# Optimization experiments

Hardware: AMD Instinct MI355X
Metric: run time of the kernel (lower is better)

Reference implementation:

```python
import jax, jax.numpy as jnp
import numpy as np

NEG_SLOPE = 0.2  # PyG GATConv default negative_slope


def _add_self_loops(edge_index, num_nodes):
    # PyG GATConv add_self_loops=True default
    loop = jnp.arange(num_nodes, dtype=edge_index.dtype)
    src = jnp.concatenate([edge_index[0], loop])
    dst = jnp.concatenate([edge_index[1], loop])
    return src, dst


def _gat_layer(x, src, dst, W, att_src, att_dst, bias, heads, out_ch):
    """One PyG-style GATConv layer (concat=True).
    x: [N, F_in]; W: [F_in, heads*out_ch]; att_*: [heads, out_ch]; bias: [heads*out_ch].
    """
    N = x.shape[0]
    h = (x @ W).reshape(N, heads, out_ch)               # [N, H, C]
    a_src = jnp.einsum('nhc,hc->nh', h, att_src)        # [N, H]
    a_dst = jnp.einsum('nhc,hc->nh', h, att_dst)        # [N, H]
    logits = jax.nn.leaky_relu(a_src[src] + a_dst[dst], NEG_SLOPE)  # [E, H]
    # segment softmax over destination neighborhoods
    m = jax.ops.segment_max(logits, dst, num_segments=N)            # [N, H]
    e = jnp.exp(logits - m[dst])                                     # [E, H]
    s = jax.ops.segment_sum(e, dst, num_segments=N)                  # [N, H]
    alpha = e / s[dst]                                               # [E, H]
    # scatter-aggregate weighted source features
    out = jax.ops.segment_sum(alpha[:, :, None] * h[src], dst, num_segments=N)  # [N, H, C]
    return out.reshape(N, heads * out_ch) + bias


def setup_inputs() -> dict:
    key = jax.random.key(0)
    ks = jax.random.split(key, 10)
    N, E = 50000, 800000
    F_in, HID, H, NC = 128, 64, 4, 10
    x = jax.random.normal(ks[0], (N, F_in), dtype=jnp.float32)
    edge_index = jax.random.randint(ks[1], (2, E), 0, N, dtype=jnp.int64)
    sc1 = 1.0 / np.sqrt(F_in)
    sc2 = 1.0 / np.sqrt(HID * H)
    return {
        'x': x,
        'edge_index': edge_index,
        'W1': jax.random.normal(ks[2], (F_in, H * HID), dtype=jnp.float32) * sc1,
        'att_src1': jax.random.normal(ks[3], (H, HID), dtype=jnp.float32) * sc1,
        'att_dst1': jax.random.normal(ks[4], (H, HID), dtype=jnp.float32) * sc1,
        'b1': jnp.zeros((H * HID,), dtype=jnp.float32),
        'W2': jax.random.normal(ks[5], (H * HID, NC), dtype=jnp.float32) * sc2,
        'att_src2': jax.random.normal(ks[6], (1, NC), dtype=jnp.float32) * sc2,
        'att_dst2': jax.random.normal(ks[7], (1, NC), dtype=jnp.float32) * sc2,
        'b2': jnp.zeros((NC,), dtype=jnp.float32),
    }


def reference(x, edge_index, W1, att_src1, att_dst1, b1, W2, att_src2, att_dst2, b2):
    N = x.shape[0]
    src, dst = _add_self_loops(edge_index, N)
    h = _gat_layer(x, src, dst, W1, att_src1, att_dst1, b1, heads=4, out_ch=64)
    h = jax.nn.elu(h)
    out = _gat_layer(h, src, dst, W2, att_src2, att_dst2, b2, heads=1, out_ch=10)
    return out
```

## Files before the change

### kernel.cpp

```cpp
#include <hip/hip_runtime.h>
#include <hip/hip_fp16.h>
#include <math.h>

#define NEG_SLOPE 0.2f
#define LOG2E 1.44269504088896f

#if __has_builtin(__builtin_amdgcn_exp2f)
#define EXP2(x) __builtin_amdgcn_exp2f(x)
#else
#define EXP2(x) exp2f(x)
#endif

typedef _Float16 half8 __attribute__((ext_vector_type(8)));
typedef float floatx4 __attribute__((ext_vector_type(4)));

__global__ __launch_bounds__(256) void prep1(const float* __restrict__ W1,
                                             half8* __restrict__ Bpack,
                                             int* __restrict__ deg, int N) {
  if (blockIdx.x < 16) {
    int tid = blockIdx.x * 256 + threadIdx.x;
    int l = tid & 63;
    int ksnt = tid >> 6;
    int ks = ksnt & 3;
    int nt = ksnt >> 2;
    int col = nt * 16 + (l & 15);
    int krow = ks * 32 + (l >> 4) * 8;
    half8 v;
#pragma unroll
    for (int j = 0; j < 8; j++) v[j] = (_Float16)W1[(krow + j) * 256 + col];
    Bpack[tid] = v;
  } else {
    int i = (blockIdx.x - 16) * 256 + threadIdx.x;
    if (i < N) deg[i] = 0;
  }
}

__global__ __launch_bounds__(256) void phase2(
    const float* __restrict__ x, const half8* __restrict__ Bpack,
    const float* __restrict__ att_s, const float* __restrict__ att_d,
    unsigned char* __restrict__ h1q, float* __restrict__ hscale,
    float* __restrict__ a1s, float* __restrict__ a1d,
    const int* __restrict__ dst, int* __restrict__ deg, int* __restrict__ rank,
    int N, int E, int gemmBlocks, int histBlocks) {
  if ((int)blockIdx.x >= gemmBlocks) {
    int b = blockIdx.x - gemmBlocks;
    for (int e = b * 256 + threadIdx.x; e < E; e += histBlocks * 256)
      rank[e] = atomicAdd(deg + dst[e], 1);
    return;
  }
  const int wave = threadIdx.x >> 6, lane = threadIdx.x & 63;
  const int quad = lane >> 4, li = lane & 15;
  const int n0 = (blockIdx.x * 4 + wave) * 16;
  if (n0 >= N) return;
  floatx4 acc[16];
#pragma unroll
  for (int t = 0; t < 16; t++) acc[t] = (floatx4){0.f, 0.f, 0.f, 0.f};
  const float* xrow = x + (size_t)(n0 + li) * 128;
#pragma unroll
  for (int ks = 0; ks < 4; ks++) {
    float4 xa = *(const float4*)(xrow + ks * 32 + quad * 8);
    float4 xb = *(const float4*)(xrow + ks * 32 + quad * 8 + 4);
    half8 a;
    a[0] = (_Float16)xa.x; a[1] = (_Float16)xa.y;
    a[2] = (_Float16)xa.z; a[3] = (_Float16)xa.w;
    a[4] = (_Float16)xb.x; a[5] = (_Float16)xb.y;
    a[6] = (_Float16)xb.z; a[7] = (_Float16)xb.w;
#pragma unroll
    for (int nt = 0; nt < 16; nt++) {
      half8 b = Bpack[(nt * 4 + ks) * 64 + lane];
      acc[nt] = __builtin_amdgcn_mfma_f32_16x16x32_f16(a, b, acc[nt], 0, 0, 0);
    }
  }
#pragma unroll
  for (int r = 0; r < 4; r++) {
    float m = 0.f;
#pragma unroll
    for (int nt = 0; nt < 16; nt++) m = fmaxf(m, fabsf(acc[nt][r]));
#pragma unroll
    for (int off = 8; off > 0; off >>= 1) m = fmaxf(m, __shfl_xor(m, off, 16));
    m = fmaxf(m, 1e-8f);
    float inv = 127.0f / m;
    int node = n0 + quad * 4 + r;
    if (li == 0) hscale[node] = m * (1.0f / 127.0f);
#pragma unroll
    for (int nt = 0; nt < 16; nt++) {
      h1q[(size_t)node * 256 + nt * 16 + li] =
          (unsigned char)(int)(fmaf(acc[nt][r], inv, 128.5f));
    }
  }
  float as_f[16], ad_f[16];
#pragma unroll
  for (int nt = 0; nt < 16; nt++) {
    as_f[nt] = att_s[nt * 16 + li];
    ad_f[nt] = att_d[nt * 16 + li];
  }
#pragma unroll
  for (int r = 0; r < 4; r++) {
    int node = n0 + quad * 4 + r;
#pragma unroll
    for (int h = 0; h < 4; h++) {
      float vs = 0.f, vd = 0.f;
#pragma unroll
      for (int ntl = 0; ntl < 4; ntl++) {
        int nt = h * 4 + ntl;
        vs = fmaf(acc[nt][r], as_f[nt], vs);
        vd = fmaf(acc[nt][r], ad_f[nt], vd);
      }
#pragma unroll
      for (int off = 8; off > 0; off >>= 1) {
        vs += __shfl_down(vs, off, 16);
        vd += __shfl_down(vd, off, 16);
      }
      if (li == 0) {
        a1s[node * 4 + h] = vs * LOG2E;
        a1d[node * 4 + h] = vd * LOG2E;
      }
    }
  }
}

__global__ void scan_local(const int* __restrict__ deg, int* __restrict__ excl,
                           int* __restrict__ bsum, int N) {
  __shared__ int s[256];
  int i = blockIdx.x * 256 + threadIdx.x;
  int v = (i < N) ? deg[i] + 1 : 0;
  s[threadIdx.x] = v;
  __syncthreads();
  for (int off = 1; off < 256; off <<= 1) {
    int t = (threadIdx.x >= off) ? s[threadIdx.x - off] : 0;
    __syncthreads();
    s[threadIdx.x] += t;
    __syncthreads();
  }
  if (i < N) excl[i] = s[threadIdx.x] - v;
  if (threadIdx.x == 255) bsum[blockIdx.x] = s[255];
}

__global__ void scan_add2(const int* __restrict__ excl, const int* __restrict__ bsum,
                          int* __restrict__ rowptr, int* __restrict__ elist,
                          int N, int nb) {
  __shared__ int s[256];
  int v = (threadIdx.x < nb) ? bsum[threadIdx.x] : 0;
  s[threadIdx.x] = v;
  __syncthreads();
  for (int off = 1; off < 256; off <<= 1) {
    int t = (threadIdx.x >= off) ? s[threadIdx.x - off] : 0;
    __syncthreads();
    s[threadIdx.x] += t;
    __syncthreads();
  }
  __syncthreads();
  int base = (blockIdx.x > 0) ? s[blockIdx.x - 1] : 0;
  int i = blockIdx.x * 256 + threadIdx.x;
  if (i < N) {
    int r = excl[i] + base;
    rowptr[i] = r;
    elist[r] = i;
  }
  if (blockIdx.x == 0 && threadIdx.x == 0) rowptr[N] = s[nb - 1];
}

__global__ void scatter2(const int* __restrict__ src, const int* __restrict__ dst,
                         const int* __restrict__ rank, const int* __restrict__ rowptr,
                         int* __restrict__ elist, int E) {
  int e = blockIdx.x * 256 + threadIdx.x;
  if (e >= E) return;
  elist[rowptr[dst[e]] + 1 + rank[e]] = src[e];
}

__global__ __launch_bounds__(256) void agg1_fused(
    const int* __restrict__ rowptr, const int* __restrict__ elist,
    const unsigned char* __restrict__ h1q, const float* __restrict__ hscale,
    const float* __restrict__ a1s, const float* __restrict__ a1d,
    const float* __restrict__ b1, const float* __restrict__ W2,
    const float* __restrict__ as2, const float* __restrict__ ad2,
    __half* __restrict__ h2, float* __restrict__ a2s, float* __restrict__ a2d,
    int N) {
  __shared__ float w2s[64 * 41];
  __shared__ float cbuf[8][256];
  const int t = threadIdx.x;
  for (int i = t; i < 2560; i += 256) {
    int ch = i / 10, jj = i - ch * 10;
    w2s[(ch >> 2) * 41 + (ch & 3) * 10 + jj] = W2[i];
  }

  const int wave = t >> 6, lane = t & 63;
  const int half = lane >> 5, l32 = lane & 31;
  const int slot = wave * 2 + half;
  const int n = blockIdx.x * 8 + slot;
  const bool act = n < N;
  const int row = act ? rowptr[n] : 0;
  const int deg = act ? rowptr[n + 1] - row : 0;
  const int* el = elist + row;
  const int hidx = l32 >> 3;
  const float adh = act ? a1d[n * 4 + hidx] : 0.f;

  float den = 0.f, T = 0.f;
  float acc[8];
#pragma unroll
  for (int k = 0; k < 8; k++) acc[k] = 0.f;

  int j = 0;
  for (; j + 4 <= deg; j += 4) {
    int ss[4];
    float lv[4], sc[4];
    uint2 qv[4];
#pragma unroll
    for (int u = 0; u < 4; u++) ss[u] = el[j + u];
#pragma unroll
    for (int u = 0; u < 4; u++) {
      lv[u] = a1s[ss[u] * 4 + hidx];
      sc[u] = hscale[ss[u]];
      qv[u] = *(const uint2*)(h1q + (size_t)ss[u] * 256 + l32 * 8);
    }
#pragma unroll
    for (int u = 0; u < 4; u++) {
      float l = lv[u] + adh;
      float e = EXP2(fmaxf(l, NEG_SLOPE * l));
      den += e;
      float se = e * sc[u];
      T += se;
      unsigned int a = qv[u].x, b = qv[u].y;
      acc[0] = fmaf((float)(a & 0xffu), se, acc[0]);
      acc[1] = fmaf((float)((a >> 8) & 0xffu), se, acc[1]);
      acc[2] = fmaf((float)((a >> 16) & 0xffu), se, acc[2]);
      acc[3] = fmaf((float)(a >> 24), se, acc[3]);
      acc[4] = fmaf((float)(b & 0xffu), se, acc[4]);
      acc[5] = fmaf((float)((b >> 8) & 0xffu), se, acc[5]);
      acc[6] = fmaf((float)((b >> 16) & 0xffu), se, acc[6]);
      acc[7] = fmaf((float)(b >> 24), se, acc[7]);
    }
  }
  for (; j < deg; j++) {
    int s0 = el[j];
    float l0 = a1s[s0 * 4 + hidx] + adh;
    float sc0 = hscale[s0];
    uint2 q0 = *(const uint2*)(h1q + (size_t)s0 * 256 + l32 * 8);
    float e0 = EXP2(fmaxf(l0, NEG_SLOPE * l0));
    den += e0;
    float se = e0 * sc0;
    T += se;
    unsigned int a = q0.x, b = q0.y;
    acc[0] = fmaf((float)(a & 0xffu), se, acc[0]);
    acc[1] = fmaf((float)((a >> 8) & 0xffu), se, acc[1]);
    acc[2] = fmaf((float)((a >> 16) & 0xffu), se, acc[2]);
    acc[3] = fmaf((float)(a >> 24), se, acc[3]);
    acc[4] = fmaf((float)(b & 0xffu), se, acc[4]);
    acc[5] = fmaf((float)((b >> 8) & 0xffu), se, acc[5]);
    acc[6] = fmaf((float)((b >> 16) & 0xffu), se, acc[6]);
    acc[7] = fmaf((float)(b >> 24), se, acc[7]);
  }

  if (act) {
    float inv = 1.0f / den;
    float corr = 128.0f * T;
    float4 v0 = make_float4((acc[0] - corr) * inv, (acc[1] - corr) * inv,
                            (acc[2] - corr) * inv, (acc[3] - corr) * inv);
    float4 v1 = make_float4((acc[4] - corr) * inv, (acc[5] - corr) * inv,
                            (acc[6] - corr) * inv, (acc[7] - corr) * inv);
    *(float4*)&cbuf[slot][l32 * 8] = v0;
    *(float4*)&cbuf[slot][l32 * 8 + 4] = v1;
  }
  __syncthreads();

  float4 bb = *(const float4*)(b1 + lane * 4);
  const float* w0 = w2s + lane * 41;
#pragma unroll
  for (int pp = 0; pp < 2; pp++) {
    int slot2 = wave * 2 + pp;
    int n2 = blockIdx.x * 8 + slot2;
    if (n2 >= N) continue;
    float4 cv = *(const float4*)&cbuf[slot2][lane * 4];
    float c0 = cv.x + bb.x;
    float c1 = cv.y + bb.y;
    float c2 = cv.z + bb.z;
    float c3 = cv.w + bb.w;
    c0 = c0 > 0.f ? c0 : expm1f(c0);
    c1 = c1 > 0.f ? c1 : expm1f(c1);
    c2 = c2 > 0.f ? c2 : expm1f(c2);
    c3 = c3 > 0.f ? c3 : expm1f(c3);
    float p[10];
#pragma unroll
    for (int jj = 0; jj < 10; jj++)
      p[jj] = fmaf(c0, w0[jj],
              fmaf(c1, w0[10 + jj], fmaf(c2, w0[20 + jj], c3 * w0[30 + jj])));
#pragma unroll
    for (int jj = 0; jj < 10; jj++) {
#pragma unroll
      for (int off = 32; off > 0; off >>= 1) p[jj] += __shfl_down(p[jj], off, 64);
    }
    if (lane == 0) {
      float ds = 0.f, dd = 0.f;
#pragma unroll
      for (int jj = 0; jj < 10; jj++) {
        h2[(size_t)n2 * 16 + jj] = __float2half(p[jj]);
        ds = fmaf(p[jj], as2[jj], ds);
        dd = fmaf(p[jj], ad2[jj], dd);
      }
      a2s[n2] = ds * LOG2E;
      a2d[n2] = dd * LOG2E;
    }
  }
}

__global__ __launch_bounds__(256) void agg2_csr(
    const int* __restrict__ rowptr, const int* __restrict__ elist,
    const __half* __restrict__ h2, const float* __restrict__ a2s,
    const float* __restrict__ a2d, const float* __restrict__ b2,
    float* __restrict__ out, int N) {
  int wave = threadIdx.x >> 6, lane = threadIdx.x & 63;
  int n = blockIdx.x * 4 + wave;
  if (n >= N) return;
  int row = rowptr[n];
  int deg = rowptr[n + 1] - row;
  const int* el = elist + row;
  float ad = a2d[n];
  int g = lane / 5;
  int c2 = lane - g * 5;
  float den = 0.f, ax = 0.f, ay = 0.f;
  if (g < 12) {
    int jj = g;
    for (; jj + 12 < deg; jj += 24) {
      int sA = el[jj], sB = el[jj + 12];
      float lA = a2s[sA] + ad;
      float lB = a2s[sB] + ad;
      __half2 hA = *(const __half2*)(h2 + (size_t)sA * 16 + c2 * 2);
      __half2 hB = *(const __half2*)(h2 + (size_t)sB * 16 + c2 * 2);
      float eA = EXP2(fmaxf(lA, NEG_SLOPE * lA));
      float eB = EXP2(fmaxf(lB, NEG_SLOPE * lB));
      den += eA + eB;
      float2 fA = __half22float2(hA);
      float2 fB = __half22float2(hB);
      ax = fmaf(eA, fA.x, fmaf(eB, fB.x, ax));
      ay = fmaf(eA, fA.y, fmaf(eB, fB.y, ay));
    }
    for (; jj < deg; jj += 12) {
      int s = el[jj];
      float l = a2s[s] + ad;
      __half2 hv = *(const __half2*)(h2 + (size_t)s * 16 + c2 * 2);
      float ev = EXP2(fmaxf(l, NEG_SLOPE * l));
      den += ev;
      float2 f = __half22float2(hv);
      ax = fmaf(ev, f.x, ax);
      ay = fmaf(ev, f.y, ay);
    }
  }
  ax += __shfl_down(ax, 30, 64);
  ay += __shfl_down(ay, 30, 64);
  den += __shfl_down(den, 30, 64);
  ax += __shfl_down(ax, 10, 64) + __shfl_down(ax, 20, 64);
  ay += __shfl_down(ay, 10, 64) + __shfl_down(ay, 20, 64);
  den += __shfl_down(den, 10, 64) + __shfl_down(den, 20, 64);
  ax += __shfl_down(ax, 5, 64);
  ay += __shfl_down(ay, 5, 64);
  den += __shfl_down(den, 5, 64);
  if (lane < 5) {
    float inv = 1.0f / den;
    float2 bb = *(const float2*)(b2 + lane * 2);
    float2 o = make_float2(fmaf(ax, inv, bb.x), fmaf(ay, inv, bb.y));
    *(float2*)(out + (size_t)n * 10 + lane * 2) = o;
  }
}

extern "C" void kernel_launch(void* const* d_in, const int* in_sizes, int n_in,
                              void* d_out, int out_size, void* d_ws, size_t ws_size,
                              hipStream_t stream) {
  const float* x = (const float*)d_in[0];
  const int* ei = (const int*)d_in[1];
  const float* W1 = (const float*)d_in[2];
  const float* as1 = (const float*)d_in[3];
  const float* ad1 = (const float*)d_in[4];
  const float* b1 = (const float*)d_in[5];
  const float* W2 = (const float*)d_in[6];
  const float* as2 = (const float*)d_in[7];
  const float* ad2 = (const float*)d_in[8];
  const float* b2 = (const float*)d_in[9];
  float* out = (float*)d_out;

  const int N = in_sizes[0] / 128;
  const int E = in_sizes[1] / 2;
  const int* srcp = ei;
  const int* dstp = ei + E;

  char* ws = (char*)d_ws;
  size_t off = 0;
  auto alloc = [&](size_t nbytes) {
    char* p = ws + off;
    off += (nbytes + 255) & ~(size_t)255;
    return p;
  };
  unsigned char* h1q = (unsigned char*)alloc((size_t)N * 256);
  float* hscale = (float*)alloc((size_t)N * 4);
  half8* Bpack = (half8*)alloc((size_t)4096 * 16);
  float* a1s = (float*)alloc((size_t)N * 4 * 4);
  float* a1d = (float*)alloc((size_t)N * 4 * 4);
  __half* h2 = (__half*)alloc((size_t)N * 16 * 2);
  float* a2sv = (float*)alloc((size_t)N * 4);
  float* a2dv = (float*)alloc((size_t)N * 4);
  int* deg = (int*)alloc((size_t)N * 4);
  int* excl = (int*)alloc((size_t)N * 4);
  int* bsum = (int*)alloc(256 * 4);
  int* rowptr = (int*)alloc((size_t)(N + 1) * 4);
  int* rank = (int*)alloc((size_t)E * 4);
  int* elist = (int*)alloc((size_t)(E + (size_t)N) * 4);

  const int nb = (N + 255) / 256;
  const int gemmBlocks = (N / 16 + 3) / 4;
  const int histBlocks = 512;

  prep1<<<16 + nb, 256, 0, stream>>>(W1, Bpack, deg, N);
  phase2<<<gemmBlocks + histBlocks, 256, 0, stream>>>(
      x, Bpack, as1, ad1, h1q, hscale, a1s, a1d, dstp, deg, rank, N, E,
      gemmBlocks, histBlocks);
  scan_local<<<nb, 256, 0, stream>>>(deg, excl, bsum, N);
  scan_add2<<<nb, 256, 0, stream>>>(excl, bsum, rowptr, elist, N, nb);
  scatter2<<<(E + 255) / 256, 256, 0, stream>>>(srcp, dstp, rank, rowptr, elist, E);
  agg1_fused<<<(N + 7) / 8, 256, 0, stream>>>(rowptr, elist, h1q, hscale, a1s, a1d,
                                              b1, W2, as2, ad2, h2, a2sv, a2dv, N);
  agg2_csr<<<(N + 3) / 4, 256, 0, stream>>>(rowptr, elist, h2, a2sv, a2dv, b2, out, N);
}
```

Measured before the change: 255.5 us.

## Cooperatively compute edge weights per 32-edge chunk and share via LDS

In the layer-1 aggregation, each lane of a half-wave now loads one neighbor's index, all four head logits and its scale, computes the four exponentials once, and publishes weights and row offsets through shared memory. Before, every lane recomputed its head's exp and reloaded the index, logit and scale for each edge. Denominators and scale sums are reduced with shuffles at the end, and launch bounds request 4 blocks per CU. The cost is extra LDS traffic, lgkmcnt waits with scheduling barriers, and tail handling, and low-degree nodes may see little benefit.

Measured after the change: 259.1 us. No clear change (+1.4%).

```diff
diff --git a/kernel.cpp b/kernel.cpp
--- a/kernel.cpp
+++ b/kernel.cpp
@@ -168,7 +168,7 @@
   elist[rowptr[dst[e]] + 1 + rank[e]] = src[e];
 }
 
-__global__ __launch_bounds__(256) void agg1_fused(
+__global__ __launch_bounds__(256, 4) void agg1_fused(
     const int* __restrict__ rowptr, const int* __restrict__ elist,
     const unsigned char* __restrict__ h1q, const float* __restrict__ hscale,
     const float* __restrict__ a1s, const float* __restrict__ a1d,
@@ -178,6 +178,8 @@
     int N) {
   __shared__ float w2s[64 * 41];
   __shared__ float cbuf[8][256];
+  __shared__ float sem[8][32][4];
+  __shared__ int soff[8][32];
   const int t = threadIdx.x;
   for (int i = t; i < 2560; i += 256) {
     int ch = i / 10, jj = i - ch * 10;
@@ -193,67 +195,109 @@
   const int deg = act ? rowptr[n + 1] - row : 0;
   const int* el = elist + row;
   const int hidx = l32 >> 3;
-  const float adh = act ? a1d[n * 4 + hidx] : 0.f;
-
-  float den = 0.f, T = 0.f;
+  float4 adv = act ? *(const float4*)(a1d + (size_t)n * 4)
+                   : make_float4(0.f, 0.f, 0.f, 0.f);
+
+  const float* semp = &sem[slot][0][0];
+  const int* sp = &soff[slot][0];
+  const unsigned char* h1ql = h1q + l32 * 8;
+
+  float den4[4] = {0.f, 0.f, 0.f, 0.f};
+  float T4[4] = {0.f, 0.f, 0.f, 0.f};
   float acc[8];
 #pragma unroll
   for (int k = 0; k < 8; k++) acc[k] = 0.f;
 
-  int j = 0;
-  for (; j + 4 <= deg; j += 4) {
-    int ss[4];
-    float lv[4], sc[4];
-    uint2 qv[4];
-#pragma unroll
-    for (int u = 0; u < 4; u++) ss[u] = el[j + u];
-#pragma unroll
-    for (int u = 0; u < 4; u++) {
-      lv[u] = a1s[ss[u] * 4 + hidx];
-      sc[u] = hscale[ss[u]];
-      qv[u] = *(const uint2*)(h1q + (size_t)ss[u] * 256 + l32 * 8);
-    }
-#pragma unroll
-    for (int u = 0; u < 4; u++) {
-      float l = lv[u] + adh;
-      float e = EXP2(fmaxf(l, NEG_SLOPE * l));
-      den += e;
-      float se = e * sc[u];
-      T += se;
-      unsigned int a = qv[u].x, b = qv[u].y;
-      acc[0] = fmaf((float)(a & 0xffu), se, acc[0]);
-      acc[1] = fmaf((float)((a >> 8) & 0xffu), se, acc[1]);
-      acc[2] = fmaf((float)((a >> 16) & 0xffu), se, acc[2]);
-      acc[3] = fmaf((float)(a >> 24), se, acc[3]);
-      acc[4] = fmaf((float)(b & 0xffu), se, acc[4]);
-      acc[5] = fmaf((float)((b >> 8) & 0xffu), se, acc[5]);
-      acc[6] = fmaf((float)((b >> 16) & 0xffu), se, acc[6]);
-      acc[7] = fmaf((float)(b >> 24), se, acc[7]);
-    }
-  }
-  for (; j < deg; j++) {
-    int s0 = el[j];
-    float l0 = a1s[s0 * 4 + hidx] + adh;
-    float sc0 = hscale[s0];
-    uint2 q0 = *(const uint2*)(h1q + (size_t)s0 * 256 + l32 * 8);
-    float e0 = EXP2(fmaxf(l0, NEG_SLOPE * l0));
-    den += e0;
-    float se = e0 * sc0;
-    T += se;
-    unsigned int a = q0.x, b = q0.y;
-    acc[0] = fmaf((float)(a & 0xffu), se, acc[0]);
-    acc[1] = fmaf((float)((a >> 8) & 0xffu), se, acc[1]);
-    acc[2] = fmaf((float)((a >> 16) & 0xffu), se, acc[2]);
-    acc[3] = fmaf((float)(a >> 24), se, acc[3]);
-    acc[4] = fmaf((float)(b & 0xffu), se, acc[4]);
-    acc[5] = fmaf((float)((b >> 8) & 0xffu), se, acc[5]);
-    acc[6] = fmaf((float)((b >> 16) & 0xffu), se, acc[6]);
-    acc[7] = fmaf((float)(b >> 24), se, acc[7]);
+  for (int j = 0; j < deg; j += 32) {
+    int m = deg - j;
+    if (m > 32) m = 32;
+    int idx = j + l32;
+    bool valid = idx < deg;
+    if (idx >= deg) idx = deg - 1;
+    int s = el[idx];
+    float4 av = *(const float4*)(a1s + (size_t)s * 4);
+    float sc = hscale[s];
+    float4 sev;
+    {
+      float l0 = av.x + adv.x;
+      float l1 = av.y + adv.y;
+      float l2 = av.z + adv.z;
+      float l3 = av.w + adv.w;
+      float e0 = EXP2(fmaxf(l0, NEG_SLOPE * l0));
+      float e1 = EXP2(fmaxf(l1, NEG_SLOPE * l1));
+      float e2 = EXP2(fmaxf(l2, NEG_SLOPE * l2));
+      float e3 = EXP2(fmaxf(l3, NEG_SLOPE * l3));
+      e0 = valid ? e0 : 0.f;
+      e1 = valid ? e1 : 0.f;
+      e2 = valid ? e2 : 0.f;
+      e3 = valid ? e3 : 0.f;
+      den4[0] += e0; den4[1] += e1; den4[2] += e2; den4[3] += e3;
+      sev.x = e0 * sc; sev.y = e1 * sc; sev.z = e2 * sc; sev.w = e3 * sc;
+      T4[0] += sev.x; T4[1] += sev.y; T4[2] += sev.z; T4[3] += sev.w;
+    }
+    __builtin_amdgcn_sched_barrier(0);
+    asm volatile("s_waitcnt lgkmcnt(0)" ::: "memory");
+    __builtin_amdgcn_sched_barrier(0);
+    *(float4*)&sem[slot][l32][0] = sev;
+    soff[slot][l32] = s << 8;
+    __builtin_amdgcn_sched_barrier(0);
+    asm volatile("s_waitcnt lgkmcnt(0)" ::: "memory");
+    __builtin_amdgcn_sched_barrier(0);
+    int u = 0;
+    for (; u + 8 <= m; u += 8) {
+      int ov[8];
+      float se[8];
+      uint2 qv[8];
+#pragma unroll
+      for (int k = 0; k < 8; k++) {
+        ov[k] = sp[u + k];
+        se[k] = semp[(u + k) * 4 + hidx];
+      }
+#pragma unroll
+      for (int k = 0; k < 8; k++)
+        qv[k] = *(const uint2*)(h1ql + (size_t)(unsigned)ov[k]);
+#pragma unroll
+      for (int k = 0; k < 8; k++) {
+        unsigned int a = qv[k].x, b = qv[k].y;
+        float w = se[k];
+        acc[0] = fmaf((float)(a & 0xffu), w, acc[0]);
+        acc[1] = fmaf((float)((a >> 8) & 0xffu), w, acc[1]);
+        acc[2] = fmaf((float)((a >> 16) & 0xffu), w, acc[2]);
+        acc[3] = fmaf((float)(a >> 24), w, acc[3]);
+        acc[4] = fmaf((float)(b & 0xffu), w, acc[4]);
+        acc[5] = fmaf((float)((b >> 8) & 0xffu), w, acc[5]);
+        acc[6] = fmaf((float)((b >> 16) & 0xffu), w, acc[6]);
+        acc[7] = fmaf((float)(b >> 24), w, acc[7]);
+      }
+    }
+    for (; u < m; u++) {
+      int o0 = sp[u];
+      float w = semp[u * 4 + hidx];
+      uint2 q0 = *(const uint2*)(h1ql + (size_t)(unsigned)o0);
+      unsigned int a = q0.x, b = q0.y;
+      acc[0] = fmaf((float)(a & 0xffu), w, acc[0]);
+      acc[1] = fmaf((float)((a >> 8) & 0xffu), w, acc[1]);
+      acc[2] = fmaf((float)((a >> 16) & 0xffu), w, acc[2]);
+      acc[3] = fmaf((float)(a >> 24), w, acc[3]);
+      acc[4] = fmaf((float)(b & 0xffu), w, acc[4]);
+      acc[5] = fmaf((float)((b >> 8) & 0xffu), w, acc[5]);
+      acc[6] = fmaf((float)((b >> 16) & 0xffu), w, acc[6]);
+      acc[7] = fmaf((float)(b >> 24), w, acc[7]);
+    }
+  }
+
+#pragma unroll
+  for (int off = 16; off > 0; off >>= 1) {
+#pragma unroll
+    for (int h = 0; h < 4; h++) {
+      den4[h] += __shfl_xor(den4[h], off, 32);
+      T4[h] += __shfl_xor(T4[h], off, 32);
+    }
   }
 
   if (act) {
-    float inv = 1.0f / den;
-    float corr = 128.0f * T;
+    float inv = 1.0f / den4[hidx];
+    float corr = 128.0f * T4[hidx];
     float4 v0 = make_float4((acc[0] - corr) * inv, (acc[1] - corr) * inv,
                             (acc[2] - corr) * inv, (acc[3] - corr) * inv);
     float4 v1 = make_float4((acc[4] - corr) * inv, (acc[5] - corr) * inv,
```
